# Kernel optimization log

Hardware: AMD Instinct MI355X
Metric: run time of the kernel (lower is better)

The kernel has to match this reference:

```python
import jax, jax.numpy as jnp
import numpy as np

N_HEAD = 10

def setup_inputs() -> dict:
    key = jax.random.key(0)
    k1, k2, k3 = jax.random.split(key, 3)
    n_embd = 640
    x = jax.random.normal(k1, (4, 2048, n_embd), dtype=jnp.float32)
    w_qkv = jax.random.normal(k2, (3 * n_embd, n_embd), dtype=jnp.float32) * (1.0 / np.sqrt(n_embd))
    w_proj = jax.random.normal(k3, (n_embd, n_embd), dtype=jnp.float32) * (1.0 / np.sqrt(n_embd))
    return {"x": x, "w_qkv": w_qkv, "w_proj": w_proj}

def reference(x, w_qkv, w_proj):
    bsz, seqlen, n_embd = x.shape
    head_dim = n_embd // N_HEAD
    qkv = jnp.einsum('bsd,ed->bse', x, w_qkv)  # [B,S,3E]
    q, k, v = jnp.split(qkv, 3, axis=2)
    # [B,H,S,Dh]
    q = q.reshape(bsz, seqlen, N_HEAD, head_dim).transpose(0, 2, 1, 3)
    k = k.reshape(bsz, seqlen, N_HEAD, head_dim).transpose(0, 2, 1, 3)
    v = v.reshape(bsz, seqlen, N_HEAD, head_dim).transpose(0, 2, 1, 3)
    scale = 1.0 / np.sqrt(head_dim).astype(np.float32)
    scores = jnp.einsum('bhqd,bhkd->bhqk', q, k) * scale
    causal = jnp.tril(jnp.ones((seqlen, seqlen), dtype=bool))
    scores = jnp.where(causal, scores, jnp.finfo(scores.dtype).min)
    attn = jax.nn.softmax(scores, axis=-1)
    y = jnp.einsum('bhqk,bhkd->bhqd', attn, v)
    y = y.transpose(0, 2, 1, 3).reshape(bsz, seqlen, n_embd)
    return jnp.einsum('bsd,ed->bse', y, w_proj)
```

## Files before the change

### kernel.cpp

```cpp
#include <hip/hip_runtime.h>

#define BB 4
#define SS 2048
#define EE 640
#define NHH 10
#define DHH 64
#define MTOK 8192
#define E33 1920

#define LDST 72

#if __has_builtin(__builtin_amdgcn_exp2f)
#define EXP2(x) __builtin_amdgcn_exp2f(x)
#else
#define EXP2(x) exp2f(x)
#endif

#define QSCALE 0.18033688011112042f

typedef float f32x4 __attribute__((ext_vector_type(4)));
typedef __bf16 bf16x8 __attribute__((ext_vector_type(8)));
typedef __bf16 bf16x4 __attribute__((ext_vector_type(4)));
typedef unsigned short u16;
typedef u16 u16x4 __attribute__((ext_vector_type(4)));

__device__ inline u16 f2bf(float f) {
  unsigned u = __builtin_bit_cast(unsigned, f);
  u += 0x7fffu + ((u >> 16) & 1u);
  return (u16)(u >> 16);
}

__global__ void convert_kernel(const float* __restrict__ in, u16* __restrict__ out, int n4) {
  int i = blockIdx.x * blockDim.x + threadIdx.x;
  if (i < n4) {
    float4 v = ((const float4*)in)[i];
    u16x4 o = { f2bf(v.x), f2bf(v.y), f2bf(v.z), f2bf(v.w) };
    ((u16x4*)out)[i] = o;
  }
}

__global__ __launch_bounds__(256) void gemm_qkv(
    const u16* __restrict__ A, const u16* __restrict__ Bt,
    u16* __restrict__ qb, u16* __restrict__ kb, u16* __restrict__ vt) {
  __shared__ __align__(16) u16 As[128 * LDST];
  __shared__ __align__(16) u16 Bs[128 * LDST];
  const int t = threadIdx.x;
  const int m0 = blockIdx.y * 128;
  const int n0 = blockIdx.x * 128;
  const int w = t >> 6, lane = t & 63, n16 = lane & 15, quad = lane >> 4;
  const int wm = w >> 1, wn = w & 1;

  f32x4 acc[4][4];
  for (int i = 0; i < 4; i++)
    for (int j = 0; j < 4; j++) acc[i][j] = f32x4{0.f, 0.f, 0.f, 0.f};

  for (int kt = 0; kt < 10; ++kt) {
    __syncthreads();
    for (int i = 0; i < 4; ++i) {
      int c = i * 256 + t;
      int row = c >> 3, col0 = (c & 7) * 8;
      *(bf16x8*)&As[row * LDST + col0] = *(const bf16x8*)&A[(m0 + row) * 640 + kt * 64 + col0];
      *(bf16x8*)&Bs[row * LDST + col0] = *(const bf16x8*)&Bt[(n0 + row) * 640 + kt * 64 + col0];
    }
    __syncthreads();
    for (int ks = 0; ks < 2; ++ks) {
      bf16x8 a[4], b[4];
      for (int mi = 0; mi < 4; mi++)
        a[mi] = *(const bf16x8*)&As[(wm * 64 + mi * 16 + n16) * LDST + ks * 32 + quad * 8];
      for (int ni = 0; ni < 4; ni++)
        b[ni] = *(const bf16x8*)&Bs[(wn * 64 + ni * 16 + n16) * LDST + ks * 32 + quad * 8];
      for (int mi = 0; mi < 4; mi++)
        for (int ni = 0; ni < 4; ni++)
          acc[mi][ni] = __builtin_amdgcn_mfma_f32_16x16x32_bf16(a[mi], b[ni], acc[mi][ni], 0, 0, 0);
    }
  }

  const int which = n0 / 640;
  for (int ni = 0; ni < 4; ni++) {
    int col = n0 + wn * 64 + ni * 16 + n16;
    int eh = col - which * 640;
    int h = eh >> 6, d = eh & 63;
    for (int mi = 0; mi < 4; mi++) {
      int tb = m0 + wm * 64 + mi * 16 + quad * 4;
      f32x4 c = acc[mi][ni];
      if (which == 0) {
        c[0] *= QSCALE; c[1] *= QSCALE; c[2] *= QSCALE; c[3] *= QSCALE;
      }
      if (which == 2) {
        int b_ = tb >> 11, s_ = tb & 2047;
        u16x4 pk = { f2bf(c[0]), f2bf(c[1]), f2bf(c[2]), f2bf(c[3]) };
        *(u16x4*)&vt[((b_ * NHH + h) * DHH + d) * SS + s_] = pk;
      } else {
        u16* dst = (which == 0) ? qb : kb;
        for (int r = 0; r < 4; r++) {
          int tok = tb + r;
          int b_ = tok >> 11, s_ = tok & 2047;
          dst[((b_ * NHH + h) * SS + s_) * DHH + d] = f2bf(c[r]);
        }
      }
    }
  }
}

__global__ __launch_bounds__(256) void attn_kernel(
    const u16* __restrict__ qb, const u16* __restrict__ kb, const u16* __restrict__ vt,
    u16* __restrict__ y) {
  __shared__ __align__(16) u16 Ks[2][64 * LDST];
  __shared__ __align__(16) u16 Vs[2][64 * LDST];
  const int t = threadIdx.x;
  const int w = t >> 6, lane = t & 63, n16 = lane & 15, quad = lane >> 4;
  const int bh = blockIdx.x;
  const int qt = 31 - blockIdx.y;
  const int qb0 = qt * 64;
  const int b_ = bh / NHH, h = bh % NHH;

  bf16x8 aq[2];
  {
    const u16* qp = &qb[(bh * SS + qb0 + w * 16 + n16) * DHH];
    aq[0] = *(const bf16x8*)&qp[quad * 8];
    aq[1] = *(const bf16x8*)&qp[32 + quad * 8];
  }
  const int q_rel = w * 16 + n16;

  const int c1 = 256 + t;
  const int row0 = t >> 3,  col0 = (t & 7) * 8;
  const int row1 = c1 >> 3, col1 = (c1 & 7) * 8;
  auto perm = [](int k) {
    int p = k >> 5, rem = k & 31, qd = rem >> 3, tt = rem & 7;
    return ((p << 1) | (tt >> 2)) * 16 + qd * 4 + (tt & 3);
  };
  const int prow0 = perm(row0), prow1 = perm(row1);

  float4 fk0, fk1, fv0, fv1;
  fk0 = *(const float4*)&kb[(bh * SS + row0) * DHH + col0];
  fk1 = *(const float4*)&kb[(bh * SS + row1) * DHH + col1];
  fv0 = *(const float4*)&vt[(bh * DHH + row0) * SS + col0];
  fv1 = *(const float4*)&vt[(bh * DHH + row1) * SS + col1];
  *(float4*)&Ks[0][prow0 * LDST + col0] = fk0;
  *(float4*)&Ks[0][prow1 * LDST + col1] = fk1;
  *(float4*)&Vs[0][row0 * LDST + col0] = fv0;
  *(float4*)&Vs[0][row1 * LDST + col1] = fv1;

  float m_i = -1e30f, l_i = 0.f;
  f32x4 o[4];
  for (int db = 0; db < 4; db++) o[db] = f32x4{0.f, 0.f, 0.f, 0.f};

  for (int kt = 0; kt <= qt; ++kt) {
    __syncthreads();
    const int cur = kt & 1, nxt = cur ^ 1;
    if (kt < qt) {
      int kk = (kt + 1) * 64;
      fk0 = *(const float4*)&kb[(bh * SS + kk + row0) * DHH + col0];
      fk1 = *(const float4*)&kb[(bh * SS + kk + row1) * DHH + col1];
      fv0 = *(const float4*)&vt[(bh * DHH + row0) * SS + kk + col0];
      fv1 = *(const float4*)&vt[(bh * DHH + row1) * SS + kk + col1];
    }

    f32x4 sc[4];
    for (int nb = 0; nb < 4; nb++) {
      f32x4 c = f32x4{0.f, 0.f, 0.f, 0.f};
      for (int ks = 0; ks < 2; ks++) {
        bf16x8 ak = *(const bf16x8*)&Ks[cur][(nb * 16 + n16) * LDST + ks * 32 + quad * 8];
        c = __builtin_amdgcn_mfma_f32_16x16x32_bf16(ak, aq[ks], c, 0, 0, 0);
      }
      sc[nb] = c;
    }
    if (kt == qt) {
      for (int nb = 0; nb < 4; nb++)
        for (int r = 0; r < 4; r++) {
          int key = ((nb >> 1) << 5) + quad * 8 + ((nb & 1) << 2) + r;
          if (key > q_rel) sc[nb][r] = -1e30f;
        }
    }

    f32x4 mx;
    for (int r = 0; r < 4; r++)
      mx[r] = fmaxf(fmaxf(sc[0][r], sc[1][r]), fmaxf(sc[2][r], sc[3][r]));
    float rm = fmaxf(fmaxf(mx[0], mx[1]), fmaxf(mx[2], mx[3]));
    rm = fmaxf(rm, __shfl_xor(rm, 16));
    rm = fmaxf(rm, __shfl_xor(rm, 32));

    if (!__all(rm - m_i <= 8.0f)) {
      float mnew = fmaxf(m_i, rm);
      float alpha = EXP2(m_i - mnew);
      l_i *= alpha;
      for (int db = 0; db < 4; db++)
        for (int r = 0; r < 4; r++) o[db][r] *= alpha;
      m_i = mnew;
    }

    f32x4 ps[4];
    for (int nb = 0; nb < 4; nb++)
      for (int r = 0; r < 4; r++) ps[nb][r] = EXP2(sc[nb][r] - m_i);
    f32x4 sv;
    for (int r = 0; r < 4; r++)
      sv[r] = (ps[0][r] + ps[1][r]) + (ps[2][r] + ps[3][r]);
    float rs = (sv[0] + sv[1]) + (sv[2] + sv[3]);
    rs += __shfl_xor(rs, 16);
    rs += __shfl_xor(rs, 32);
    l_i += rs;

    for (int p2 = 0; p2 < 2; p2++) {
      bf16x8 bp;
      for (int j = 0; j < 4; j++) {
        bp[j]     = (__bf16)ps[2 * p2][j];
        bp[4 + j] = (__bf16)ps[2 * p2 + 1][j];
      }
      for (int db = 0; db < 4; db++) {
        bf16x8 av = *(const bf16x8*)&Vs[cur][(db * 16 + n16) * LDST + p2 * 32 + quad * 8];
        o[db] = __builtin_amdgcn_mfma_f32_16x16x32_bf16(av, bp, o[db], 0, 0, 0);
      }
    }

    if (kt < qt) {
      *(float4*)&Ks[nxt][prow0 * LDST + col0] = fk0;
      *(float4*)&Ks[nxt][prow1 * LDST + col1] = fk1;
      *(float4*)&Vs[nxt][row0 * LDST + col0] = fv0;
      *(float4*)&Vs[nxt][row1 * LDST + col1] = fv1;
    }
  }

  const float inv = 1.0f / l_i;
  const int tok = b_ * SS + qb0 + w * 16 + n16;
  for (int db = 0; db < 4; db++) {
    bf16x4 pk = { (__bf16)(o[db][0] * inv), (__bf16)(o[db][1] * inv),
                  (__bf16)(o[db][2] * inv), (__bf16)(o[db][3] * inv) };
    *(bf16x4*)&y[tok * EE + h * DHH + db * 16 + quad * 4] = pk;
  }
}

__global__ __launch_bounds__(256) void gemm_proj(
    const u16* __restrict__ A, const u16* __restrict__ Bt, float* __restrict__ out) {
  __shared__ __align__(16) u16 As[128 * LDST];
  __shared__ __align__(16) u16 Bs[128 * LDST];
  const int t = threadIdx.x;
  const int m0 = blockIdx.y * 128;
  const int n0 = blockIdx.x * 128;
  const int w = t >> 6, lane = t & 63, n16 = lane & 15, quad = lane >> 4;
  const int wm = w >> 1, wn = w & 1;

  f32x4 acc[4][4];
  for (int i = 0; i < 4; i++)
    for (int j = 0; j < 4; j++) acc[i][j] = f32x4{0.f, 0.f, 0.f, 0.f};

  for (int kt = 0; kt < 10; ++kt) {
    __syncthreads();
    for (int i = 0; i < 4; ++i) {
      int c = i * 256 + t;
      int row = c >> 3, col0 = (c & 7) * 8;
      *(bf16x8*)&As[row * LDST + col0] = *(const bf16x8*)&A[(m0 + row) * 640 + kt * 64 + col0];
      *(bf16x8*)&Bs[row * LDST + col0] = *(const bf16x8*)&Bt[(n0 + row) * 640 + kt * 64 + col0];
    }
    __syncthreads();
    for (int ks = 0; ks < 2; ++ks) {
      bf16x8 a[4], b[4];
      for (int mi = 0; mi < 4; mi++)
        a[mi] = *(const bf16x8*)&As[(wm * 64 + mi * 16 + n16) * LDST + ks * 32 + quad * 8];
      for (int ni = 0; ni < 4; ni++)
        b[ni] = *(const bf16x8*)&Bs[(wn * 64 + ni * 16 + n16) * LDST + ks * 32 + quad * 8];
      for (int mi = 0; mi < 4; mi++)
        for (int ni = 0; ni < 4; ni++)
          acc[mi][ni] = __builtin_amdgcn_mfma_f32_16x16x32_bf16(a[mi], b[ni], acc[mi][ni], 0, 0, 0);
    }
  }

  for (int ni = 0; ni < 4; ni++) {
    int col = n0 + wn * 64 + ni * 16 + n16;
    for (int mi = 0; mi < 4; mi++) {
      int rowb = m0 + wm * 64 + mi * 16 + quad * 4;
      f32x4 c = acc[mi][ni];
      for (int r = 0; r < 4; r++) out[(rowb + r) * 640 + col] = c[r];
    }
  }
}

extern "C" void kernel_launch(void* const* d_in, const int* in_sizes, int n_in,
                              void* d_out, int out_size, void* d_ws, size_t ws_size,
                              hipStream_t stream) {
  const float* x     = (const float*)d_in[0];
  const float* wqkv  = (const float*)d_in[1];
  const float* wproj = (const float*)d_in[2];
  float* out = (float*)d_out;

  char* ws = (char*)d_ws;
  u16* xb     = (u16*)(ws + 0);
  u16* wqkvb  = (u16*)(ws + 10485760);
  u16* wprojb = (u16*)(ws + 12943360);
  u16* qbuf   = (u16*)(ws + 13762560);
  u16* kbuf   = (u16*)(ws + 24248320);
  u16* vtb    = (u16*)(ws + 34734080);
  u16* ybuf   = (u16*)(ws + 45219840);

  convert_kernel<<<5120, 256, 0, stream>>>(x, xb, 5242880 / 4);
  convert_kernel<<<1200, 256, 0, stream>>>(wqkv, wqkvb, 1228800 / 4);
  convert_kernel<<<400, 256, 0, stream>>>(wproj, wprojb, 409600 / 4);

  gemm_qkv<<<dim3(15, 64), 256, 0, stream>>>(xb, wqkvb, qbuf, kbuf, vtb);
  attn_kernel<<<dim3(40, 32), 256, 0, stream>>>(qbuf, kbuf, vtb, ybuf);
  gemm_proj<<<dim3(5, 64), 256, 0, stream>>>(ybuf, wprojb, out);
}
```

Baseline: 179.8 us.

## Process 128 query rows per attention block, reusing each K/V tile twice

Each attention block now handles a 128-row query tile, with every wave owning two 16-row query slices, instead of a 64-row tile. Each K/V tile loaded into shared memory is reused by twice as many MFMA ops, which halves K/V global traffic and shared-memory staging per query. Causal masking is now applied per slice based on the key offset. The cost is higher register pressure from doubled accumulators and half as many blocks (640), which may reduce occupancy, add tail imbalance, and waste some masked work on the diagonal tiles.

```diff
diff --git a/kernel.cpp b/kernel.cpp
--- a/kernel.cpp
+++ b/kernel.cpp
@@ -110,17 +110,18 @@
   const int t = threadIdx.x;
   const int w = t >> 6, lane = t & 63, n16 = lane & 15, quad = lane >> 4;
   const int bh = blockIdx.x;
-  const int qt = 31 - blockIdx.y;
-  const int qb0 = qt * 64;
+  const int qt = 15 - blockIdx.y;
+  const int qb0 = qt * 128;
   const int b_ = bh / NHH, h = bh % NHH;
-
-  bf16x8 aq[2];
-  {
-    const u16* qp = &qb[(bh * SS + qb0 + w * 16 + n16) * DHH];
-    aq[0] = *(const bf16x8*)&qp[quad * 8];
-    aq[1] = *(const bf16x8*)&qp[32 + quad * 8];
-  }
-  const int q_rel = w * 16 + n16;
+  const int qlo = w * 32;
+
+  bf16x8 aq[2][2];
+#pragma unroll
+  for (int qh = 0; qh < 2; qh++) {
+    const u16* qp = &qb[(bh * SS + qb0 + qlo + qh * 16 + n16) * DHH];
+    aq[qh][0] = *(const bf16x8*)&qp[quad * 8];
+    aq[qh][1] = *(const bf16x8*)&qp[32 + quad * 8];
+  }
 
   const int c1 = 256 + t;
   const int row0 = t >> 3,  col0 = (t & 7) * 8;
@@ -141,14 +142,18 @@
   *(float4*)&Vs[0][row0 * LDST + col0] = fv0;
   *(float4*)&Vs[0][row1 * LDST + col1] = fv1;
 
-  float m_i = -1e30f, l_i = 0.f;
-  f32x4 o[4];
-  for (int db = 0; db < 4; db++) o[db] = f32x4{0.f, 0.f, 0.f, 0.f};
-
-  for (int kt = 0; kt <= qt; ++kt) {
+  float m_i[2] = {-1e30f, -1e30f}, l_i[2] = {0.f, 0.f};
+  f32x4 o[2][4];
+#pragma unroll
+  for (int qh = 0; qh < 2; qh++)
+    for (int db = 0; db < 4; db++) o[qh][db] = f32x4{0.f, 0.f, 0.f, 0.f};
+
+  const int nt = 2 * qt + 2;
+
+  for (int kt = 0; kt < nt; ++kt) {
     __syncthreads();
     const int cur = kt & 1, nxt = cur ^ 1;
-    if (kt < qt) {
+    if (kt < nt - 1) {
       int kk = (kt + 1) * 64;
       fk0 = *(const float4*)&kb[(bh * SS + kk + row0) * DHH + col0];
       fk1 = *(const float4*)&kb[(bh * SS + kk + row1) * DHH + col1];
@@ -156,63 +161,91 @@
       fv1 = *(const float4*)&vt[(bh * DHH + row1) * SS + kk + col1];
     }
 
-    f32x4 sc[4];
+    f32x4 sc[2][4];
+#pragma unroll
     for (int nb = 0; nb < 4; nb++) {
-      f32x4 c = f32x4{0.f, 0.f, 0.f, 0.f};
+      f32x4 c0 = f32x4{0.f, 0.f, 0.f, 0.f};
+      f32x4 c1 = f32x4{0.f, 0.f, 0.f, 0.f};
+#pragma unroll
       for (int ks = 0; ks < 2; ks++) {
         bf16x8 ak = *(const bf16x8*)&Ks[cur][(nb * 16 + n16) * LDST + ks * 32 + quad * 8];
-        c = __builtin_amdgcn_mfma_f32_16x16x32_bf16(ak, aq[ks], c, 0, 0, 0);
-      }
-      sc[nb] = c;
-    }
-    if (kt == qt) {
+        c0 = __builtin_amdgcn_mfma_f32_16x16x32_bf16(ak, aq[0][ks], c0, 0, 0, 0);
+        c1 = __builtin_amdgcn_mfma_f32_16x16x32_bf16(ak, aq[1][ks], c1, 0, 0, 0);
+      }
+      sc[0][nb] = c0; sc[1][nb] = c1;
+    }
+
+    const int koff = kt * 64 - 128 * qt;
+    f32x4 ps[2][4];
+    bf16x8 bp[2][2];
+#pragma unroll
+    for (int qh = 0; qh < 2; qh++) {
+      if (koff + 63 > qlo + qh * 16) {
+        const int qrel = qlo + qh * 16 + n16;
+#pragma unroll
+        for (int nb = 0; nb < 4; nb++)
+#pragma unroll
+          for (int r = 0; r < 4; r++) {
+            int key = koff + ((nb >> 1) << 5) + quad * 8 + ((nb & 1) << 2) + r;
+            if (key > qrel) sc[qh][nb][r] = -1e30f;
+          }
+      }
+
+      f32x4 mx;
+#pragma unroll
+      for (int r = 0; r < 4; r++)
+        mx[r] = fmaxf(fmaxf(sc[qh][0][r], sc[qh][1][r]), fmaxf(sc[qh][2][r], sc[qh][3][r]));
+      float rm = fmaxf(fmaxf(mx[0], mx[1]), fmaxf(mx[2], mx[3]));
+      rm = fmaxf(rm, __shfl_xor(rm, 16));
+      rm = fmaxf(rm, __shfl_xor(rm, 32));
+
+      if (!__all(rm - m_i[qh] <= 8.0f)) {
+        float mnew = fmaxf(m_i[qh], rm);
+        float alpha = EXP2(m_i[qh] - mnew);
+        l_i[qh] *= alpha;
+#pragma unroll
+        for (int db = 0; db < 4; db++)
+#pragma unroll
+          for (int r = 0; r < 4; r++) o[qh][db][r] *= alpha;
+        m_i[qh] = mnew;
+      }
+
+#pragma unroll
       for (int nb = 0; nb < 4; nb++)
-        for (int r = 0; r < 4; r++) {
-          int key = ((nb >> 1) << 5) + quad * 8 + ((nb & 1) << 2) + r;
-          if (key > q_rel) sc[nb][r] = -1e30f;
+#pragma unroll
+        for (int r = 0; r < 4; r++) ps[qh][nb][r] = EXP2(sc[qh][nb][r] - m_i[qh]);
+      f32x4 sv;
+#pragma unroll
+      for (int r = 0; r < 4; r++)
+        sv[r] = (ps[qh][0][r] + ps[qh][1][r]) + (ps[qh][2][r] + ps[qh][3][r]);
+      float rs = (sv[0] + sv[1]) + (sv[2] + sv[3]);
+      rs += __shfl_xor(rs, 16);
+      rs += __shfl_xor(rs, 32);
+      l_i[qh] += rs;
+
+#pragma unroll
+      for (int p2 = 0; p2 < 2; p2++) {
+        bf16x8 b;
+#pragma unroll
+        for (int j = 0; j < 4; j++) {
+          b[j]     = (__bf16)ps[qh][2 * p2][j];
+          b[4 + j] = (__bf16)ps[qh][2 * p2 + 1][j];
         }
-    }
-
-    f32x4 mx;
-    for (int r = 0; r < 4; r++)
-      mx[r] = fmaxf(fmaxf(sc[0][r], sc[1][r]), fmaxf(sc[2][r], sc[3][r]));
-    float rm = fmaxf(fmaxf(mx[0], mx[1]), fmaxf(mx[2], mx[3]));
-    rm = fmaxf(rm, __shfl_xor(rm, 16));
-    rm = fmaxf(rm, __shfl_xor(rm, 32));
-
-    if (!__all(rm - m_i <= 8.0f)) {
-      float mnew = fmaxf(m_i, rm);
-      float alpha = EXP2(m_i - mnew);
-      l_i *= alpha;
-      for (int db = 0; db < 4; db++)
-        for (int r = 0; r < 4; r++) o[db][r] *= alpha;
-      m_i = mnew;
-    }
-
-    f32x4 ps[4];
-    for (int nb = 0; nb < 4; nb++)
-      for (int r = 0; r < 4; r++) ps[nb][r] = EXP2(sc[nb][r] - m_i);
-    f32x4 sv;
-    for (int r = 0; r < 4; r++)
-      sv[r] = (ps[0][r] + ps[1][r]) + (ps[2][r] + ps[3][r]);
-    float rs = (sv[0] + sv[1]) + (sv[2] + sv[3]);
-    rs += __shfl_xor(rs, 16);
-    rs += __shfl_xor(rs, 32);
-    l_i += rs;
-
+        bp[qh][p2] = b;
+      }
+    }
+
+#pragma unroll
     for (int p2 = 0; p2 < 2; p2++) {
-      bf16x8 bp;
-      for (int j = 0; j < 4; j++) {
-        bp[j]     = (__bf16)ps[2 * p2][j];
-        bp[4 + j] = (__bf16)ps[2 * p2 + 1][j];
-      }
+#pragma unroll
       for (int db = 0; db < 4; db++) {
         bf16x8 av = *(const bf16x8*)&Vs[cur][(db * 16 + n16) * LDST + p2 * 32 + quad * 8];
-        o[db] = __builtin_amdgcn_mfma_f32_16x16x32_bf16(av, bp, o[db], 0, 0, 0);
-      }
-    }
-
-    if (kt < qt) {
+        o[0][db] = __builtin_amdgcn_mfma_f32_16x16x32_bf16(av, bp[0][p2], o[0][db], 0, 0, 0);
+        o[1][db] = __builtin_amdgcn_mfma_f32_16x16x32_bf16(av, bp[1][p2], o[1][db], 0, 0, 0);
+      }
+    }
+
+    if (kt < nt - 1) {
       *(float4*)&Ks[nxt][prow0 * LDST + col0] = fk0;
       *(float4*)&Ks[nxt][prow1 * LDST + col1] = fk1;
       *(float4*)&Vs[nxt][row0 * LDST + col0] = fv0;
@@ -220,12 +253,16 @@
     }
   }
 
-  const float inv = 1.0f / l_i;
-  const int tok = b_ * SS + qb0 + w * 16 + n16;
-  for (int db = 0; db < 4; db++) {
-    bf16x4 pk = { (__bf16)(o[db][0] * inv), (__bf16)(o[db][1] * inv),
-                  (__bf16)(o[db][2] * inv), (__bf16)(o[db][3] * inv) };
-    *(bf16x4*)&y[tok * EE + h * DHH + db * 16 + quad * 4] = pk;
+#pragma unroll
+  for (int qh = 0; qh < 2; qh++) {
+    const float inv = 1.0f / l_i[qh];
+    const int tok = b_ * SS + qb0 + qlo + qh * 16 + n16;
+#pragma unroll
+    for (int db = 0; db < 4; db++) {
+      bf16x4 pk = { (__bf16)(o[qh][db][0] * inv), (__bf16)(o[qh][db][1] * inv),
+                    (__bf16)(o[qh][db][2] * inv), (__bf16)(o[qh][db][3] * inv) };
+      *(bf16x4*)&y[tok * EE + h * DHH + db * 16 + quad * 4] = pk;
+    }
   }
 }
 
@@ -296,6 +333,6 @@
   convert_kernel<<<400, 256, 0, stream>>>(wproj, wprojb, 409600 / 4);
 
   gemm_qkv<<<dim3(15, 64), 256, 0, stream>>>(xb, wqkvb, qbuf, kbuf, vtb);
-  attn_kernel<<<dim3(40, 32), 256, 0, stream>>>(qbuf, kbuf, vtb, ybuf);
+  attn_kernel<<<dim3(40, 16), 256, 0, stream>>>(qbuf, kbuf, vtb, ybuf);
   gemm_proj<<<dim3(5, 64), 256, 0, stream>>>(ybuf, wprojb, out);
 }
```

Measured after the change: 192.5 us. 1.07x slower.

## Load V fragments directly from global memory into registers, dropping LDS staging

Applied to the files above, without the earlier changes.

The attention kernel no longer stages V tiles through shared memory. Each lane now reads its bf16x8 V fragments straight from global memory (the transposed vt layout) at the start of every key tile. This removes the V shared-memory writes and reads and halves LDS use per block, which may raise occupancy. The cost is that all four waves redundantly fetch the same V data from global/L2 each tile, with no prefetch overlap, so latency may be exposed. Unroll pragmas are also added to the inner loops.

```diff
diff --git a/kernel.cpp b/kernel.cpp
--- a/kernel.cpp
+++ b/kernel.cpp
@@ -106,7 +106,6 @@
     const u16* __restrict__ qb, const u16* __restrict__ kb, const u16* __restrict__ vt,
     u16* __restrict__ y) {
   __shared__ __align__(16) u16 Ks[2][64 * LDST];
-  __shared__ __align__(16) u16 Vs[2][64 * LDST];
   const int t = threadIdx.x;
   const int w = t >> 6, lane = t & 63, n16 = lane & 15, quad = lane >> 4;
   const int bh = blockIdx.x;
@@ -131,15 +130,13 @@
   };
   const int prow0 = perm(row0), prow1 = perm(row1);
 
-  float4 fk0, fk1, fv0, fv1;
+  float4 fk0, fk1;
   fk0 = *(const float4*)&kb[(bh * SS + row0) * DHH + col0];
   fk1 = *(const float4*)&kb[(bh * SS + row1) * DHH + col1];
-  fv0 = *(const float4*)&vt[(bh * DHH + row0) * SS + col0];
-  fv1 = *(const float4*)&vt[(bh * DHH + row1) * SS + col1];
   *(float4*)&Ks[0][prow0 * LDST + col0] = fk0;
   *(float4*)&Ks[0][prow1 * LDST + col1] = fk1;
-  *(float4*)&Vs[0][row0 * LDST + col0] = fv0;
-  *(float4*)&Vs[0][row1 * LDST + col1] = fv1;
+
+  const u16* vbase = &vt[((size_t)bh * DHH + n16) * SS + quad * 8];
 
   float m_i = -1e30f, l_i = 0.f;
   f32x4 o[4];
@@ -148,25 +145,35 @@
   for (int kt = 0; kt <= qt; ++kt) {
     __syncthreads();
     const int cur = kt & 1, nxt = cur ^ 1;
+    const int kk = kt * 64;
+
+    bf16x8 av[2][4];
+#pragma unroll
+    for (int p2 = 0; p2 < 2; p2++)
+#pragma unroll
+      for (int db = 0; db < 4; db++)
+        av[p2][db] = *(const bf16x8*)&vbase[(size_t)db * 16 * SS + kk + p2 * 32];
+
     if (kt < qt) {
-      int kk = (kt + 1) * 64;
-      fk0 = *(const float4*)&kb[(bh * SS + kk + row0) * DHH + col0];
-      fk1 = *(const float4*)&kb[(bh * SS + kk + row1) * DHH + col1];
-      fv0 = *(const float4*)&vt[(bh * DHH + row0) * SS + kk + col0];
-      fv1 = *(const float4*)&vt[(bh * DHH + row1) * SS + kk + col1];
+      fk0 = *(const float4*)&kb[(bh * SS + kk + 64 + row0) * DHH + col0];
+      fk1 = *(const float4*)&kb[(bh * SS + kk + 64 + row1) * DHH + col1];
     }
 
     f32x4 sc[4];
+#pragma unroll
     for (int nb = 0; nb < 4; nb++) {
       f32x4 c = f32x4{0.f, 0.f, 0.f, 0.f};
-      for (int ks = 0; ks < 2; ks++) {
-        bf16x8 ak = *(const bf16x8*)&Ks[cur][(nb * 16 + n16) * LDST + ks * 32 + quad * 8];
-        c = __builtin_amdgcn_mfma_f32_16x16x32_bf16(ak, aq[ks], c, 0, 0, 0);
-      }
+      bf16x8 ak0 = *(const bf16x8*)&Ks[cur][(nb * 16 + n16) * LDST + quad * 8];
+      c = __builtin_amdgcn_mfma_f32_16x16x32_bf16(ak0, aq[0], c, 0, 0, 0);
+      bf16x8 ak1 = *(const bf16x8*)&Ks[cur][(nb * 16 + n16) * LDST + 32 + quad * 8];
+      c = __builtin_amdgcn_mfma_f32_16x16x32_bf16(ak1, aq[1], c, 0, 0, 0);
       sc[nb] = c;
     }
+
     if (kt == qt) {
+#pragma unroll
       for (int nb = 0; nb < 4; nb++)
+#pragma unroll
         for (int r = 0; r < 4; r++) {
           int key = ((nb >> 1) << 5) + quad * 8 + ((nb & 1) << 2) + r;
           if (key > q_rel) sc[nb][r] = -1e30f;
@@ -174,6 +181,7 @@
     }
 
     f32x4 mx;
+#pragma unroll
     for (int r = 0; r < 4; r++)
       mx[r] = fmaxf(fmaxf(sc[0][r], sc[1][r]), fmaxf(sc[2][r], sc[3][r]));
     float rm = fmaxf(fmaxf(mx[0], mx[1]), fmaxf(mx[2], mx[3]));
@@ -184,15 +192,20 @@
       float mnew = fmaxf(m_i, rm);
       float alpha = EXP2(m_i - mnew);
       l_i *= alpha;
+#pragma unroll
       for (int db = 0; db < 4; db++)
+#pragma unroll
         for (int r = 0; r < 4; r++) o[db][r] *= alpha;
       m_i = mnew;
     }
 
     f32x4 ps[4];
+#pragma unroll
     for (int nb = 0; nb < 4; nb++)
+#pragma unroll
       for (int r = 0; r < 4; r++) ps[nb][r] = EXP2(sc[nb][r] - m_i);
     f32x4 sv;
+#pragma unroll
     for (int r = 0; r < 4; r++)
       sv[r] = (ps[0][r] + ps[1][r]) + (ps[2][r] + ps[3][r]);
     float rs = (sv[0] + sv[1]) + (sv[2] + sv[3]);
@@ -200,28 +213,28 @@
     rs += __shfl_xor(rs, 32);
     l_i += rs;
 
+#pragma unroll
     for (int p2 = 0; p2 < 2; p2++) {
       bf16x8 bp;
+#pragma unroll
       for (int j = 0; j < 4; j++) {
         bp[j]     = (__bf16)ps[2 * p2][j];
         bp[4 + j] = (__bf16)ps[2 * p2 + 1][j];
       }
-      for (int db = 0; db < 4; db++) {
-        bf16x8 av = *(const bf16x8*)&Vs[cur][(db * 16 + n16) * LDST + p2 * 32 + quad * 8];
-        o[db] = __builtin_amdgcn_mfma_f32_16x16x32_bf16(av, bp, o[db], 0, 0, 0);
-      }
+#pragma unroll
+      for (int db = 0; db < 4; db++)
+        o[db] = __builtin_amdgcn_mfma_f32_16x16x32_bf16(av[p2][db], bp, o[db], 0, 0, 0);
     }
 
     if (kt < qt) {
       *(float4*)&Ks[nxt][prow0 * LDST + col0] = fk0;
       *(float4*)&Ks[nxt][prow1 * LDST + col1] = fk1;
-      *(float4*)&Vs[nxt][row0 * LDST + col0] = fv0;
-      *(float4*)&Vs[nxt][row1 * LDST + col1] = fv1;
     }
   }
 
   const float inv = 1.0f / l_i;
   const int tok = b_ * SS + qb0 + w * 16 + n16;
+#pragma unroll
   for (int db = 0; db < 4; db++) {
     bf16x4 pk = { (__bf16)(o[db][0] * inv), (__bf16)(o[db][1] * inv),
                   (__bf16)(o[db][2] * inv), (__bf16)(o[db][3] * inv) };
```

Result: slower. 226.8 us (+26.1%).

## Register-prefetch next K tile in GEMMs and merge conversion launches

Applied to the files above, without the earlier changes.

Both GEMM kernels now load the next K-slice from global memory into registers while MFMAs run on the current shared-memory tile, so global load latency overlaps compute. The three fp32-to-bf16 conversion launches become one kernel that picks its source by index, removing two launches. The attention loop gains unroll pragmas and splits its two QK MFMA loads by hand. Holding the prefetched tile in registers raises register pressure and may lower occupancy.

```diff
diff --git a/kernel.cpp b/kernel.cpp
--- a/kernel.cpp
+++ b/kernel.cpp
@@ -30,13 +30,22 @@
   return (u16)(u >> 16);
 }
 
-__global__ void convert_kernel(const float* __restrict__ in, u16* __restrict__ out, int n4) {
+#define XN4   1310720
+#define WQN4   307200
+#define WPN4   102400
+__global__ void convert_all(const float* __restrict__ x, const float* __restrict__ wqkv,
+                            const float* __restrict__ wproj,
+                            u16* __restrict__ xb, u16* __restrict__ wqkvb,
+                            u16* __restrict__ wprojb) {
   int i = blockIdx.x * blockDim.x + threadIdx.x;
-  if (i < n4) {
-    float4 v = ((const float4*)in)[i];
-    u16x4 o = { f2bf(v.x), f2bf(v.y), f2bf(v.z), f2bf(v.w) };
-    ((u16x4*)out)[i] = o;
-  }
+  const float* src; u16* dst; int off;
+  if (i < XN4)              { src = x;     dst = xb;     off = i; }
+  else if (i < XN4 + WQN4)  { src = wqkv;  dst = wqkvb;  off = i - XN4; }
+  else if (i < XN4 + WQN4 + WPN4) { src = wproj; dst = wprojb; off = i - XN4 - WQN4; }
+  else return;
+  float4 v = ((const float4*)src)[off];
+  u16x4 o = { f2bf(v.x), f2bf(v.y), f2bf(v.z), f2bf(v.w) };
+  ((u16x4*)dst)[off] = o;
 }
 
 __global__ __launch_bounds__(256) void gemm_qkv(
@@ -54,15 +63,32 @@
   for (int i = 0; i < 4; i++)
     for (int j = 0; j < 4; j++) acc[i][j] = f32x4{0.f, 0.f, 0.f, 0.f};
 
+  bf16x8 pa[4], pb[4];
+#pragma unroll
+  for (int i = 0; i < 4; ++i) {
+    int c = i * 256 + t, row = c >> 3, col0 = (c & 7) * 8;
+    pa[i] = *(const bf16x8*)&A[(m0 + row) * 640 + col0];
+    pb[i] = *(const bf16x8*)&Bt[(n0 + row) * 640 + col0];
+  }
+
   for (int kt = 0; kt < 10; ++kt) {
     __syncthreads();
+#pragma unroll
     for (int i = 0; i < 4; ++i) {
-      int c = i * 256 + t;
-      int row = c >> 3, col0 = (c & 7) * 8;
-      *(bf16x8*)&As[row * LDST + col0] = *(const bf16x8*)&A[(m0 + row) * 640 + kt * 64 + col0];
-      *(bf16x8*)&Bs[row * LDST + col0] = *(const bf16x8*)&Bt[(n0 + row) * 640 + kt * 64 + col0];
-    }
-    __syncthreads();
+      int c = i * 256 + t, row = c >> 3, col0 = (c & 7) * 8;
+      *(bf16x8*)&As[row * LDST + col0] = pa[i];
+      *(bf16x8*)&Bs[row * LDST + col0] = pb[i];
+    }
+    __syncthreads();
+    if (kt < 9) {
+#pragma unroll
+      for (int i = 0; i < 4; ++i) {
+        int c = i * 256 + t, row = c >> 3, col0 = (c & 7) * 8;
+        pa[i] = *(const bf16x8*)&A[(m0 + row) * 640 + (kt + 1) * 64 + col0];
+        pb[i] = *(const bf16x8*)&Bt[(n0 + row) * 640 + (kt + 1) * 64 + col0];
+      }
+    }
+#pragma unroll
     for (int ks = 0; ks < 2; ++ks) {
       bf16x8 a[4], b[4];
       for (int mi = 0; mi < 4; mi++)
@@ -157,16 +183,20 @@
     }
 
     f32x4 sc[4];
+#pragma unroll
     for (int nb = 0; nb < 4; nb++) {
       f32x4 c = f32x4{0.f, 0.f, 0.f, 0.f};
-      for (int ks = 0; ks < 2; ks++) {
-        bf16x8 ak = *(const bf16x8*)&Ks[cur][(nb * 16 + n16) * LDST + ks * 32 + quad * 8];
-        c = __builtin_amdgcn_mfma_f32_16x16x32_bf16(ak, aq[ks], c, 0, 0, 0);
-      }
+      bf16x8 ak0 = *(const bf16x8*)&Ks[cur][(nb * 16 + n16) * LDST + quad * 8];
+      c = __builtin_amdgcn_mfma_f32_16x16x32_bf16(ak0, aq[0], c, 0, 0, 0);
+      bf16x8 ak1 = *(const bf16x8*)&Ks[cur][(nb * 16 + n16) * LDST + 32 + quad * 8];
+      c = __builtin_amdgcn_mfma_f32_16x16x32_bf16(ak1, aq[1], c, 0, 0, 0);
       sc[nb] = c;
     }
+
     if (kt == qt) {
+#pragma unroll
       for (int nb = 0; nb < 4; nb++)
+#pragma unroll
         for (int r = 0; r < 4; r++) {
           int key = ((nb >> 1) << 5) + quad * 8 + ((nb & 1) << 2) + r;
           if (key > q_rel) sc[nb][r] = -1e30f;
@@ -174,6 +204,7 @@
     }
 
     f32x4 mx;
+#pragma unroll
     for (int r = 0; r < 4; r++)
       mx[r] = fmaxf(fmaxf(sc[0][r], sc[1][r]), fmaxf(sc[2][r], sc[3][r]));
     float rm = fmaxf(fmaxf(mx[0], mx[1]), fmaxf(mx[2], mx[3]));
@@ -184,15 +215,20 @@
       float mnew = fmaxf(m_i, rm);
       float alpha = EXP2(m_i - mnew);
       l_i *= alpha;
+#pragma unroll
       for (int db = 0; db < 4; db++)
+#pragma unroll
         for (int r = 0; r < 4; r++) o[db][r] *= alpha;
       m_i = mnew;
     }
 
     f32x4 ps[4];
+#pragma unroll
     for (int nb = 0; nb < 4; nb++)
+#pragma unroll
       for (int r = 0; r < 4; r++) ps[nb][r] = EXP2(sc[nb][r] - m_i);
     f32x4 sv;
+#pragma unroll
     for (int r = 0; r < 4; r++)
       sv[r] = (ps[0][r] + ps[1][r]) + (ps[2][r] + ps[3][r]);
     float rs = (sv[0] + sv[1]) + (sv[2] + sv[3]);
@@ -200,12 +236,15 @@
     rs += __shfl_xor(rs, 32);
     l_i += rs;
 
+#pragma unroll
     for (int p2 = 0; p2 < 2; p2++) {
       bf16x8 bp;
+#pragma unroll
       for (int j = 0; j < 4; j++) {
         bp[j]     = (__bf16)ps[2 * p2][j];
         bp[4 + j] = (__bf16)ps[2 * p2 + 1][j];
       }
+#pragma unroll
       for (int db = 0; db < 4; db++) {
         bf16x8 av = *(const bf16x8*)&Vs[cur][(db * 16 + n16) * LDST + p2 * 32 + quad * 8];
         o[db] = __builtin_amdgcn_mfma_f32_16x16x32_bf16(av, bp, o[db], 0, 0, 0);
@@ -222,6 +261,7 @@
 
   const float inv = 1.0f / l_i;
   const int tok = b_ * SS + qb0 + w * 16 + n16;
+#pragma unroll
   for (int db = 0; db < 4; db++) {
     bf16x4 pk = { (__bf16)(o[db][0] * inv), (__bf16)(o[db][1] * inv),
                   (__bf16)(o[db][2] * inv), (__bf16)(o[db][3] * inv) };
@@ -243,15 +283,32 @@
   for (int i = 0; i < 4; i++)
     for (int j = 0; j < 4; j++) acc[i][j] = f32x4{0.f, 0.f, 0.f, 0.f};
 
+  bf16x8 pa[4], pb[4];
+#pragma unroll
+  for (int i = 0; i < 4; ++i) {
+    int c = i * 256 + t, row = c >> 3, col0 = (c & 7) * 8;
+    pa[i] = *(const bf16x8*)&A[(m0 + row) * 640 + col0];
+    pb[i] = *(const bf16x8*)&Bt[(n0 + row) * 640 + col0];
+  }
+
   for (int kt = 0; kt < 10; ++kt) {
     __syncthreads();
+#pragma unroll
     for (int i = 0; i < 4; ++i) {
-      int c = i * 256 + t;
-      int row = c >> 3, col0 = (c & 7) * 8;
-      *(bf16x8*)&As[row * LDST + col0] = *(const bf16x8*)&A[(m0 + row) * 640 + kt * 64 + col0];
-      *(bf16x8*)&Bs[row * LDST + col0] = *(const bf16x8*)&Bt[(n0 + row) * 640 + kt * 64 + col0];
-    }
-    __syncthreads();
+      int c = i * 256 + t, row = c >> 3, col0 = (c & 7) * 8;
+      *(bf16x8*)&As[row * LDST + col0] = pa[i];
+      *(bf16x8*)&Bs[row * LDST + col0] = pb[i];
+    }
+    __syncthreads();
+    if (kt < 9) {
+#pragma unroll
+      for (int i = 0; i < 4; ++i) {
+        int c = i * 256 + t, row = c >> 3, col0 = (c & 7) * 8;
+        pa[i] = *(const bf16x8*)&A[(m0 + row) * 640 + (kt + 1) * 64 + col0];
+        pb[i] = *(const bf16x8*)&Bt[(n0 + row) * 640 + (kt + 1) * 64 + col0];
+      }
+    }
+#pragma unroll
     for (int ks = 0; ks < 2; ++ks) {
       bf16x8 a[4], b[4];
       for (int mi = 0; mi < 4; mi++)
@@ -291,9 +348,7 @@
   u16* vtb    = (u16*)(ws + 34734080);
   u16* ybuf   = (u16*)(ws + 45219840);
 
-  convert_kernel<<<5120, 256, 0, stream>>>(x, xb, 5242880 / 4);
-  convert_kernel<<<1200, 256, 0, stream>>>(wqkv, wqkvb, 1228800 / 4);
-  convert_kernel<<<400, 256, 0, stream>>>(wproj, wprojb, 409600 / 4);
+  convert_all<<<6720, 256, 0, stream>>>(x, wqkv, wproj, xb, wqkvb, wprojb);
 
   gemm_qkv<<<dim3(15, 64), 256, 0, stream>>>(xb, wqkvb, qbuf, kbuf, vtb);
   attn_kernel<<<dim3(40, 32), 256, 0, stream>>>(qbuf, kbuf, vtb, ybuf);
```

After: 173.5 us. 1.04x faster.
